# Kernel optimization log

Measured on AMD Instinct MI355X. Metric: run time of the kernel, lower is better.

Reference implementation:

```python
import jax, jax.numpy as jnp
import numpy as np

# graph sizes
N_CLL, B_CLL, NODES_PER_CLL, E_CLL = 120000, 200, 600, 1200000
N_MOL, E_MOL = 64, 256
N_BIO, E_BIO = 19000, 600000
CLL_F, MOL_F, BIO_F = 128, 64, 128
H, MOL_LL, BIO_LL, CLL_LL = 200, 128, 128, 256


def _w(k, shape):
    return jax.random.normal(k, shape, dtype=jnp.float32) * 0.05


def setup_inputs() -> dict:
    key = jax.random.key(0)
    k = jax.random.split(key, 32)
    inp = {
        'x_cll': jax.random.normal(k[0], (N_CLL, CLL_F), dtype=jnp.float32),
        'x_mol': jax.random.normal(k[1], (N_MOL, MOL_F), dtype=jnp.float32),
        'x_bio': jax.random.normal(k[2], (N_BIO, BIO_F), dtype=jnp.float32),
        'edge_cll': jax.random.randint(k[3], (2, E_CLL), 0, N_CLL, dtype=jnp.int32),
        'batch_cll': (jnp.arange(N_CLL, dtype=jnp.int32) // NODES_PER_CLL),
        'edge_mol': jax.random.randint(k[4], (2, E_MOL), 0, N_MOL, dtype=jnp.int32),
        'edge_bio': jax.random.randint(k[5], (2, E_BIO), 0, N_BIO, dtype=jnp.int32),
        # cll branch (GCNConv x2 + Linear)
        'Wc1': _w(k[6], (CLL_F, H)), 'bc1': _w(k[7], (H,)),
        'Wc2': _w(k[8], (H, H)), 'bc2': _w(k[9], (H,)),
        'Wlc': _w(k[10], (H, CLL_LL)), 'blc': _w(k[11], (CLL_LL,)),
        # mol branch (GraphConv x2 + Linear)
        'Wrel1': _w(k[12], (MOL_F, H)), 'brel1': _w(k[13], (H,)), 'Wroot1': _w(k[14], (MOL_F, H)),
        'Wrel2': _w(k[15], (H, H)), 'brel2': _w(k[16], (H,)), 'Wroot2': _w(k[17], (H, H)),
        'Wlm': _w(k[18], (H, MOL_LL)), 'blm': _w(k[19], (MOL_LL,)),
        # bio branch (GCNConv x2 + Linear)
        'Wb1': _w(k[20], (BIO_F, H)), 'bb1': _w(k[21], (H,)),
        'Wb2': _w(k[22], (H, H)), 'bb2': _w(k[23], (H,)),
        'Wlb': _w(k[24], (H, BIO_LL)), 'blb': _w(k[25], (BIO_LL,)),
        # bilinear score
        'W': _w(k[26], (CLL_LL, MOL_LL + BIO_LL)),
        'bias': _w(k[27], (1,)),
    }
    return inp


def gcn_conv(x, src, dst, W, b, n):
    # PyG GCNConv: h = X W; out = D^-1/2 (A+I) D^-1/2 h + b
    h = x @ W
    loop = jnp.arange(n, dtype=src.dtype)
    s = jnp.concatenate([src, loop])
    d = jnp.concatenate([dst, loop])
    deg = jax.ops.segment_sum(jnp.ones(s.shape[0], h.dtype), d, num_segments=n)
    dinv = jax.lax.rsqrt(deg)  # deg >= 1 due to self loops
    norm = dinv[s] * dinv[d]
    return jax.ops.segment_sum(h[s] * norm[:, None], d, num_segments=n) + b


def graph_conv(x, src, dst, Wrel, brel, Wroot, n):
    # PyG GraphConv (aggr='add'): out_i = Wrel * sum_{j->i} x_j + brel + Wroot * x_i
    agg = jax.ops.segment_sum(x[src], dst, num_segments=n)
    return agg @ Wrel + brel + x @ Wroot


def mean_pool(x, batch, num_graphs):
    sums = jax.ops.segment_sum(x, batch, num_segments=num_graphs)
    cnt = jax.ops.segment_sum(jnp.ones(x.shape[0], x.dtype), batch, num_segments=num_graphs)
    return sums / cnt[:, None]


def reference(x_cll, x_mol, x_bio, edge_cll, batch_cll, edge_mol, edge_bio,
              Wc1, bc1, Wc2, bc2, Wlc, blc,
              Wrel1, brel1, Wroot1, Wrel2, brel2, Wroot2, Wlm, blm,
              Wb1, bb1, Wb2, bb2, Wlb, blb, W, bias):
    relu = jax.nn.relu
    # cell-line branch
    h = relu(gcn_conv(x_cll, edge_cll[0], edge_cll[1], Wc1, bc1, N_CLL))
    h = relu(gcn_conv(h, edge_cll[0], edge_cll[1], Wc2, bc2, N_CLL))
    xc = mean_pool(h, batch_cll, B_CLL) @ Wlc + blc  # [B_CLL, CLL_LL]
    # molecule branch (single graph -> batch of 1)
    m = relu(graph_conv(x_mol, edge_mol[0], edge_mol[1], Wrel1, brel1, Wroot1, N_MOL))
    m = relu(graph_conv(m, edge_mol[0], edge_mol[1], Wrel2, brel2, Wroot2, N_MOL))
    xm = jnp.mean(m, axis=0, keepdims=True) @ Wlm + blm  # [1, MOL_LL]
    # bio (PPI) branch: uses only the last node's embedding
    bnodes = relu(gcn_conv(x_bio, edge_bio[0], edge_bio[1], Wb1, bb1, N_BIO))
    bnodes = relu(gcn_conv(bnodes, edge_bio[0], edge_bio[1], Wb2, bb2, N_BIO))
    xb = bnodes[-1].reshape(1, -1) @ Wlb + blb  # [1, BIO_LL]
    # bilinear score
    x_drug = jnp.concatenate([xm, xb], axis=1)  # [1, MOL_LL+BIO_LL]
    scores = (xc @ W) @ x_drug.T + bias  # [B_CLL, 1]
    return scores
```

## Files before the change

### kernel.cpp

```cpp
#include <hip/hip_runtime.h>

typedef unsigned short u16;
typedef __attribute__((ext_vector_type(8))) short s16x8;
typedef __attribute__((ext_vector_type(4))) float f32x4;
typedef __attribute__((ext_vector_type(4))) unsigned u32x4;
typedef __attribute__((ext_vector_type(2))) unsigned u32x2;

#define N_CLLN 120000
#define B_CLLN 200
#define NPG    600
#define E_CLLN 1200000
#define N_MOLN 64
#define E_MOLN 256
#define N_BION 19000
#define E_BION 600000
#define NTOT   (N_CLLN + N_BION)
#define ETOT   (E_CLLN + E_BION)
#define HDIM   200
#define NT     13
#define FCAP   2048

__device__ __forceinline__ float b2f(u16 u){ return __uint_as_float(((unsigned)u)<<16); }
__device__ __forceinline__ float u2f_lo(unsigned u){ return __uint_as_float(u<<16); }
__device__ __forceinline__ float u2f_hi(unsigned u){ return __uint_as_float(u & 0xFFFF0000u); }
__device__ __forceinline__ u16 f2b(float f){
  unsigned x = __float_as_uint(f);
  return (u16)((x + 0x7fffu + ((x>>16)&1u)) >> 16);
}

__global__ void hist_all(const int* __restrict__ eC, const int* __restrict__ eB,
                         int* __restrict__ cnt, int* __restrict__ eidx){
  int i = blockIdx.x*blockDim.x + threadIdx.x;
  if (i < E_CLLN)      eidx[i] = atomicAdd(&cnt[eC[E_CLLN + i]], 1);
  else if (i < ETOT)   eidx[i] = atomicAdd(&cnt[N_CLLN + eB[E_BION + (i - E_CLLN)]], 1);
}
__global__ void make_dinv(const int* __restrict__ cnt, float* __restrict__ dinv, int N){
  int i = blockIdx.x*blockDim.x + threadIdx.x;
  if (i < N) dinv[i] = rsqrtf((float)cnt[i] + 1.0f);
}
__global__ void scan1(const int* __restrict__ cnt, int* __restrict__ rows,
                      int* __restrict__ bsum, int N){
  __shared__ int sh[256];
  int b = blockIdx.x, t = threadIdx.x;
  int base = b*1024 + t*4;
  int v[4]; int s = 0;
#pragma unroll
  for (int i=0;i<4;i++){ int idx = base+i; v[i] = (idx<N)?cnt[idx]:0; s += v[i]; }
  sh[t] = s; __syncthreads();
  for (int off=1; off<256; off<<=1){
    int x = (t>=off)? sh[t-off] : 0; __syncthreads();
    sh[t] += x; __syncthreads();
  }
  int run = (t==0)? 0 : sh[t-1];
#pragma unroll
  for (int i=0;i<4;i++){ int idx = base+i; if (idx<N) rows[idx] = run; run += v[i]; }
  if (t==255) bsum[b] = sh[255];
}
__global__ void scan2(int* __restrict__ bsum, int nb){
  __shared__ int sh[256];
  int t = threadIdx.x;
  sh[t] = (t<nb)? bsum[t] : 0; __syncthreads();
  for (int off=1; off<256; off<<=1){
    int x = (t>=off)? sh[t-off] : 0; __syncthreads();
    sh[t] += x; __syncthreads();
  }
  if (t<nb) bsum[t] = (t==0)? 0 : sh[t-1];
}
__global__ void scan3(int* __restrict__ rows, const int* __restrict__ bsum, int N){
  int i = blockIdx.x*blockDim.x + threadIdx.x;
  if (i<N) rows[i] += bsum[i>>10];
}
__global__ void scatter_all(const int* __restrict__ eC, const int* __restrict__ eB,
                            const int* __restrict__ rows, const int* __restrict__ eidx,
                            int* __restrict__ csr){
  int i = blockIdx.x*blockDim.x + threadIdx.x;
  if (i < E_CLLN){
    int d = eC[E_CLLN + i];
    csr[rows[d] + eidx[i]] = eC[i];
  } else if (i < ETOT){
    int j = i - E_CLLN;
    int d = N_CLLN + eB[E_BION + j];
    csr[rows[d] + eidx[i]] = eB[j];
  }
}

__global__ void prescale128(const float* __restrict__ x, const float* __restrict__ dinv,
                            u16* __restrict__ out, int N){
  int idx = blockIdx.x*blockDim.x + threadIdx.x;
  if (idx >= N*16) return;
  int r = idx >> 4, c8 = (idx & 15) << 3;
  float dv = dinv[r];
  const float* p = x + (size_t)r*128 + c8;
  f32x4 v0 = *(const f32x4*)p;
  f32x4 v1 = *(const f32x4*)(p+4);
  u32x4 w;
  w[0] = (unsigned)f2b(v0[0]*dv) | ((unsigned)f2b(v0[1]*dv)<<16);
  w[1] = (unsigned)f2b(v0[2]*dv) | ((unsigned)f2b(v0[3]*dv)<<16);
  w[2] = (unsigned)f2b(v1[0]*dv) | ((unsigned)f2b(v1[1]*dv)<<16);
  w[3] = (unsigned)f2b(v1[2]*dv) | ((unsigned)f2b(v1[3]*dv)<<16);
  *(u32x4*)(out + (size_t)r*128 + c8) = w;
}

__global__ __launch_bounds__(256) void gather128(
    const u16* __restrict__ X, const float* __restrict__ dinv,
    const int* __restrict__ rows, const int* __restrict__ csr,
    u16* __restrict__ Y, int N, int E)
{
  int wid = (blockIdx.x*blockDim.x + threadIdx.x) >> 6;
  int l = threadIdx.x & 63;
  if (wid >= N) return;
  int half = l >> 5, lh = l & 31;
  float dv = dinv[wid];
  int e0 = rows[wid];
  int e1 = (wid+1 < N) ? rows[wid+1] : E;
  const unsigned* base = (const unsigned*)X;
  float a0=0.f, a1=0.f, a2=0.f, a3=0.f;
  if (half == 0){
    u32x2 sv = *((const u32x2*)(base + (size_t)wid*64) + lh);
    a0 = u2f_lo(sv[0]); a1 = u2f_hi(sv[0]);
    a2 = u2f_lo(sv[1]); a3 = u2f_hi(sv[1]);
  }
  for (int b0 = e0; b0 < e1; b0 += 64){
    int n = e1 - b0;
    int cnt = n < 64 ? n : 64;
    int myv = (l < cnt) ? csr[b0 + l] : 0;
    int i = 0;
    for (; i + 15 < cnt; i += 16){
      u32x2 P[8];
#pragma unroll
      for (int u=0;u<8;u++){
        int s = __shfl(myv, i + 2*u + half);
        P[u] = *((const u32x2*)(base + (size_t)s*64) + lh);
      }
#pragma unroll
      for (int u=0;u<8;u++){
        a0 += u2f_lo(P[u][0]); a1 += u2f_hi(P[u][0]);
        a2 += u2f_lo(P[u][1]); a3 += u2f_hi(P[u][1]);
      }
    }
    for (; i < cnt; i += 2){
      int idx = i + half;
      int cidx = idx < cnt ? idx : cnt-1;
      int s = __shfl(myv, cidx);
      u32x2 P = *((const u32x2*)(base + (size_t)s*64) + lh);
      if (idx < cnt){
        a0 += u2f_lo(P[0]); a1 += u2f_hi(P[0]);
        a2 += u2f_lo(P[1]); a3 += u2f_hi(P[1]);
      }
    }
  }
  a0 += __shfl_xor(a0, 32); a1 += __shfl_xor(a1, 32);
  a2 += __shfl_xor(a2, 32); a3 += __shfl_xor(a3, 32);
  if (half == 0){
    u32x2 wv;
    wv[0] = (unsigned)f2b(a0*dv) | ((unsigned)f2b(a1*dv) << 16);
    wv[1] = (unsigned)f2b(a2*dv) | ((unsigned)f2b(a3*dv) << 16);
    *((u32x2*)((unsigned*)Y + (size_t)wid*64) + lh) = wv;
  }
}

__global__ __launch_bounds__(256) void gather200(
    const u16* __restrict__ t, const float* __restrict__ dinv,
    const int* __restrict__ rows, const int* __restrict__ csr,
    u16* __restrict__ out, int N, int E)
{
  int wid = (blockIdx.x*blockDim.x + threadIdx.x) >> 6;
  int l = threadIdx.x & 63;
  if (wid >= N) return;
  int half = l >> 5, lh = l & 31;
  bool act = lh < 25;
  float dv = dinv[wid];
  int e0 = rows[wid];
  int e1 = (wid+1 < N) ? rows[wid+1] : E;
  const unsigned* base = (const unsigned*)t;
  float a0=0.f,a1=0.f,a2=0.f,a3=0.f,a4=0.f,a5=0.f,a6=0.f,a7=0.f;
  if (half == 0 && act){
    u32x4 sv = *((const u32x4*)(base + (size_t)wid*100) + lh);
    a0 = u2f_lo(sv[0]); a1 = u2f_hi(sv[0]);
    a2 = u2f_lo(sv[1]); a3 = u2f_hi(sv[1]);
    a4 = u2f_lo(sv[2]); a5 = u2f_hi(sv[2]);
    a6 = u2f_lo(sv[3]); a7 = u2f_hi(sv[3]);
  }
  for (int b0 = e0; b0 < e1; b0 += 64){
    int n = e1 - b0;
    int cnt = n < 64 ? n : 64;
    int myv = (l < cnt) ? csr[b0 + l] : 0;
    int i = 0;
    for (; i + 15 < cnt; i += 16){
      int ss[8];
#pragma unroll
      for (int u=0;u<8;u++) ss[u] = __shfl(myv, i + 2*u + half);
      u32x4 P[8];
#pragma unroll
      for (int u=0;u<8;u++){
        u32x4 z = {0,0,0,0};
        P[u] = act ? *((const u32x4*)(base + (size_t)ss[u]*100) + lh) : z;
      }
#pragma unroll
      for (int u=0;u<8;u++){
        a0 += u2f_lo(P[u][0]); a1 += u2f_hi(P[u][0]);
        a2 += u2f_lo(P[u][1]); a3 += u2f_hi(P[u][1]);
        a4 += u2f_lo(P[u][2]); a5 += u2f_hi(P[u][2]);
        a6 += u2f_lo(P[u][3]); a7 += u2f_hi(P[u][3]);
      }
    }
    for (; i < cnt; i += 2){
      int idx = i + half;
      int cidx = idx < cnt ? idx : cnt-1;
      int s = __shfl(myv, cidx);
      u32x4 P = {0,0,0,0};
      if (act) P = *((const u32x4*)(base + (size_t)s*100) + lh);
      if (idx < cnt){
        a0 += u2f_lo(P[0]); a1 += u2f_hi(P[0]);
        a2 += u2f_lo(P[1]); a3 += u2f_hi(P[1]);
        a4 += u2f_lo(P[2]); a5 += u2f_hi(P[2]);
        a6 += u2f_lo(P[3]); a7 += u2f_hi(P[3]);
      }
    }
  }
  a0 += __shfl_xor(a0, 32); a1 += __shfl_xor(a1, 32);
  a2 += __shfl_xor(a2, 32); a3 += __shfl_xor(a3, 32);
  a4 += __shfl_xor(a4, 32); a5 += __shfl_xor(a5, 32);
  a6 += __shfl_xor(a6, 32); a7 += __shfl_xor(a7, 32);
  if (half == 0 && act){
    u32x4 wv;
    wv[0] = (unsigned)f2b(a0*dv) | ((unsigned)f2b(a1*dv) << 16);
    wv[1] = (unsigned)f2b(a2*dv) | ((unsigned)f2b(a3*dv) << 16);
    wv[2] = (unsigned)f2b(a4*dv) | ((unsigned)f2b(a5*dv) << 16);
    wv[3] = (unsigned)f2b(a6*dv) | ((unsigned)f2b(a7*dv) << 16);
    *((u32x4*)((unsigned*)out + (size_t)wid*100) + lh) = wv;
  }
}

__device__ __forceinline__ void pack_one(const float* W, u16* Bp, int K, int idx){
  int l  = idx & 63;
  int nt = (idx >> 6) % NT;
  int kk = idx / (64*NT);
  int n  = nt*16 + (l & 15);
  int k0 = kk*32 + (l>>4)*8;
  u16 v[8];
#pragma unroll
  for (int e=0;e<8;e++){
    int k = k0 + e;
    v[e] = (k < K && n < HDIM) ? f2b(W[(size_t)k*HDIM + n]) : (u16)0;
  }
#pragma unroll
  for (int e=0;e<8;e++) Bp[(size_t)idx*8 + e] = v[e];
}
__global__ void pack_both(const float* __restrict__ Wc1, u16* __restrict__ Pc1,
                          const float* __restrict__ Wc2, u16* __restrict__ Pc2){
  int idx = blockIdx.x*blockDim.x + threadIdx.x;
  const int t1 = 4*NT*64;
  if (idx < t1) pack_one(Wc1, Pc1, 128, idx);
  else if (idx < t1 + 7*NT*64) pack_one(Wc2, Pc2, 200, idx - t1);
}

template<int KSTEPS, int KACT>
__global__ __launch_bounds__(256) void gemm_h1(
    const u16* __restrict__ A, const u16* __restrict__ Bp,
    const float* __restrict__ bias, const float* __restrict__ dinv,
    u16* __restrict__ Out, int M, int Astride)
{
  const int w  = threadIdx.x >> 6;
  const int l  = threadIdx.x & 63;
  const int lm = l & 15;
  const int kg = l >> 4;
  const int base = blockIdx.x*128;
  int r0 = base + w*16 + lm;
  int r1 = r0 + 64;
  const u16* A0 = A + (size_t)(r0 < M ? r0 : 0) * Astride;
  const u16* A1 = A + (size_t)(r1 < M ? r1 : 0) * Astride;
  f32x4 acc[2][NT] = {};
  const s16x8 az = {0,0,0,0,0,0,0,0};
#pragma unroll
  for (int kk=0; kk<KSTEPS; ++kk){
    int k0 = kk*32 + kg*8;
    s16x8 a0 = (k0 < KACT) ? *(const s16x8*)(A0 + k0) : az;
    s16x8 a1 = (k0 < KACT) ? *(const s16x8*)(A1 + k0) : az;
    const u16* bp = Bp + ((size_t)kk*NT*64 + l)*8;
#pragma unroll
    for (int t=0;t<NT;t++){
      s16x8 b = *(const s16x8*)(bp + t*512);
      acc[0][t] = __builtin_amdgcn_mfma_f32_16x16x32_bf16(a0, b, acc[0][t], 0, 0, 0);
      acc[1][t] = __builtin_amdgcn_mfma_f32_16x16x32_bf16(a1, b, acc[1][t], 0, 0, 0);
    }
  }
#pragma unroll
  for (int m=0;m<2;m++){
    int orow = base + m*64 + w*16 + kg*4;
    float scj[4];
#pragma unroll
    for (int j=0;j<4;j++){ int r = orow + j; scj[j] = (r < M) ? dinv[r] : 0.f; }
#pragma unroll
    for (int t=0;t<NT;t++){
      int c = t*16 + lm;
      if (c < HDIM){
#pragma unroll
        for (int j=0;j<4;j++){
          int r = orow + j;
          if (r < M){
            float v = fmaxf(acc[m][t][j] + bias[c], 0.f) * scj[j];
            Out[(size_t)r*HDIM + c] = f2b(v);
          }
        }
      }
    }
  }
}

template<int KSTEPS, int KACT>
__global__ __launch_bounds__(256) void gemm_pool(
    const u16* __restrict__ A, const u16* __restrict__ Bp,
    const float* __restrict__ bias, float* __restrict__ pooled,
    int M, int Astride)
{
  __shared__ float ps[4][2][HDIM+8];
  for (int i = threadIdx.x; i < 4*2*(HDIM+8); i += 256) ((float*)ps)[i] = 0.f;
  __syncthreads();
  const int w  = threadIdx.x >> 6;
  const int l  = threadIdx.x & 63;
  const int lm = l & 15;
  const int kg = l >> 4;
  const int base = blockIdx.x*128;
  int r0 = base + w*16 + lm;
  int r1 = r0 + 64;
  const u16* A0 = A + (size_t)(r0 < M ? r0 : 0) * Astride;
  const u16* A1 = A + (size_t)(r1 < M ? r1 : 0) * Astride;
  f32x4 acc[2][NT] = {};
  const s16x8 az = {0,0,0,0,0,0,0,0};
#pragma unroll
  for (int kk=0; kk<KSTEPS; ++kk){
    int k0 = kk*32 + kg*8;
    s16x8 a0 = (k0 < KACT) ? *(const s16x8*)(A0 + k0) : az;
    s16x8 a1 = (k0 < KACT) ? *(const s16x8*)(A1 + k0) : az;
    const u16* bp = Bp + ((size_t)kk*NT*64 + l)*8;
#pragma unroll
    for (int t=0;t<NT;t++){
      s16x8 b = *(const s16x8*)(bp + t*512);
      acc[0][t] = __builtin_amdgcn_mfma_f32_16x16x32_bf16(a0, b, acc[0][t], 0, 0, 0);
      acc[1][t] = __builtin_amdgcn_mfma_f32_16x16x32_bf16(a1, b, acc[1][t], 0, 0, 0);
    }
  }
  const int g0 = base / NPG;
#pragma unroll
  for (int m=0;m<2;m++){
    int R0 = base + m*64 + w*16;
    bool uni = (R0 + 15 < M) && ((R0/NPG) == ((R0+15)/NPG));
    int slotU = (R0/NPG) - g0;
#pragma unroll
    for (int t=0;t<NT;t++){
      int c = t*16 + lm;
      if (c < HDIM){
        float v0 = fmaxf(acc[m][t][0] + bias[c], 0.f);
        float v1 = fmaxf(acc[m][t][1] + bias[c], 0.f);
        float v2 = fmaxf(acc[m][t][2] + bias[c], 0.f);
        float v3 = fmaxf(acc[m][t][3] + bias[c], 0.f);
        if (uni){
          float s = v0+v1+v2+v3;
          s += __shfl_xor(s, 16);
          s += __shfl_xor(s, 32);
          if (kg == 0) ps[w][slotU][c] += s;
        } else {
          float s0 = 0.f, s1 = 0.f;
          float vv[4] = {v0,v1,v2,v3};
#pragma unroll
          for (int j=0;j<4;j++){
            int r = R0 + kg*4 + j;
            if (r < M){
              if ((r/NPG) - g0 == 0) s0 += vv[j]; else s1 += vv[j];
            }
          }
          s0 += __shfl_xor(s0, 16); s0 += __shfl_xor(s0, 32);
          s1 += __shfl_xor(s1, 16); s1 += __shfl_xor(s1, 32);
          if (kg == 0){ ps[w][0][c] += s0; ps[w][1][c] += s1; }
        }
      }
    }
  }
  __syncthreads();
  for (int i = threadIdx.x; i < 2*HDIM; i += 256){
    int slot = i / HDIM, c = i % HDIM;
    float s = ps[0][slot][c] + ps[1][slot][c] + ps[2][slot][c] + ps[3][slot][c];
    int g = g0 + slot;
    if (g < B_CLLN && s != 0.f) unsafeAtomicAdd(&pooled[g*HDIM + c], s);
  }
}

__global__ void xc_kernel(const float* __restrict__ pooled, const float* __restrict__ Wlc,
                          const float* __restrict__ blc, float* __restrict__ xc){
  __shared__ float p[HDIM];
  int b = blockIdx.x, j = threadIdx.x;
  if (j < HDIM) p[j] = pooled[b*HDIM + j] * (1.0f/NPG);
  __syncthreads();
  float s = blc[j];
  for (int k=0;k<HDIM;k++) s += p[k]*Wlc[(size_t)k*256 + j];
  xc[(size_t)b*256 + j] = s;
}

__global__ void bio_front(const float* __restrict__ x_bio, const float* __restrict__ dinvAll,
                          const int* __restrict__ rowAll, const int* __restrict__ csr,
                          float* __restrict__ Y1f, float* __restrict__ dvF){
  const float* dinvB = dinvAll + N_CLLN;
  int g0l = rowAll[NTOT - 1];
  int fcnt = (ETOT - g0l) + 1; if (fcnt > FCAP) fcnt = FCAP;
  int wid = (blockIdx.x*blockDim.x + threadIdx.x) >> 6;
  int nw  = (gridDim.x*blockDim.x) >> 6;
  int l = threadIdx.x & 63;
  for (int k = wid; k < fcnt; k += nw){
    int v = (k == 0) ? (N_BION - 1) : csr[g0l + k - 1];
    float dv = dinvB[v];
    int e0 = rowAll[N_CLLN + v];
    int e1 = (v + 1 < N_BION) ? rowAll[N_CLLN + v + 1] : ETOT;
    float c0 = x_bio[(size_t)v*128 + l]      * dv;
    float c1 = x_bio[(size_t)v*128 + l + 64] * dv;
    for (int e = e0; e < e1; ++e){
      int s = csr[e];
      float ds = dinvB[s];
      c0 += x_bio[(size_t)s*128 + l]      * ds;
      c1 += x_bio[(size_t)s*128 + l + 64] * ds;
    }
    Y1f[(size_t)k*128 + l]      = c0 * dv;
    Y1f[(size_t)k*128 + l + 64] = c1 * dv;
    if (l == 0) dvF[k] = dv;
  }
}

__global__ __launch_bounds__(256) void bio_h1acc(
    const float* __restrict__ Y1f, const float* __restrict__ dvF,
    const int* __restrict__ rowAll,
    const float* __restrict__ Wb1, const float* __restrict__ bb1,
    float* __restrict__ Y2acc){
  __shared__ float y1[128];
  int tid = threadIdx.x;
  int g0l = rowAll[NTOT - 1];
  int fcnt = (ETOT - g0l) + 1; if (fcnt > FCAP) fcnt = FCAP;
  for (int k = blockIdx.x; k < fcnt; k += gridDim.x){
    if (tid < 128) y1[tid] = Y1f[(size_t)k*128 + tid];
    __syncthreads();
    if (tid < HDIM){
      float s = bb1[tid];
#pragma unroll 8
      for (int q=0;q<128;q++) s += y1[q]*Wb1[q*HDIM + tid];
      unsafeAtomicAdd(&Y2acc[tid], fmaxf(s, 0.f)*dvF[k]);
    }
    __syncthreads();
  }
}

__global__ void bio_fin(const float* __restrict__ Y2acc, const float* __restrict__ dinvAll,
                        const float* __restrict__ Wb2, const float* __restrict__ bb2,
                        const float* __restrict__ Wlb, const float* __restrict__ blb,
                        float* __restrict__ xb){
  __shared__ float Y2[HDIM];
  __shared__ float wv[HDIM];
  int tid = threadIdx.x;
  float dl = dinvAll[NTOT - 1];
  if (tid < HDIM) Y2[tid] = Y2acc[tid] * dl;
  __syncthreads();
  if (tid < HDIM){
    float s = bb2[tid];
#pragma unroll 8
    for (int q=0;q<HDIM;q++) s += Y2[q]*Wb2[q*HDIM + tid];
    wv[tid] = fmaxf(s, 0.f);
  }
  __syncthreads();
  if (tid < 128){
    float s = blb[tid];
#pragma unroll 8
    for (int c=0;c<HDIM;c++) s += wv[c]*Wlb[c*128 + tid];
    xb[tid] = s;
  }
}

__global__ void mol_agg(const float* __restrict__ x, const int* __restrict__ src,
                        const int* __restrict__ dst, float* __restrict__ a, int E, int F){
  int idx = blockIdx.x*blockDim.x + threadIdx.x;
  if (idx >= E*F) return;
  int e = idx / F, f = idx % F;
  unsafeAtomicAdd(&a[dst[e]*F + f], x[(size_t)src[e]*F + f]);
}
__global__ void mol_l1(const float* __restrict__ x, const float* __restrict__ a1,
                       const float* __restrict__ Wrel, const float* __restrict__ brel,
                       const float* __restrict__ Wroot, float* __restrict__ m1){
  int idx = blockIdx.x*blockDim.x + threadIdx.x;
  if (idx >= N_MOLN*HDIM) return;
  int i = idx / HDIM, c = idx % HDIM;
  float s = brel[c];
  for (int k=0;k<64;k++){
    s += a1[i*64+k]*Wrel[k*HDIM+c];
    s += x[i*64+k]*Wroot[k*HDIM+c];
  }
  m1[idx] = fmaxf(s, 0.f);
}
__global__ void mol_l2(const float* __restrict__ m1, const float* __restrict__ a2,
                       const float* __restrict__ Wrel2, const float* __restrict__ brel2,
                       const float* __restrict__ Wroot2, float* __restrict__ colsum){
  int idx = blockIdx.x*blockDim.x + threadIdx.x;
  if (idx >= N_MOLN*HDIM) return;
  int i = idx / HDIM, c = idx % HDIM;
  float s = brel2[c];
  for (int k=0;k<HDIM;k++){
    s += a2[i*HDIM+k]*Wrel2[k*HDIM+c] + m1[i*HDIM+k]*Wroot2[k*HDIM+c];
  }
  s = fmaxf(s, 0.f);
  unsafeAtomicAdd(&colsum[c], s*(1.0f/N_MOLN));
}
__global__ void mol_head(const float* __restrict__ colsum, const float* __restrict__ Wlm,
                         const float* __restrict__ blm, float* __restrict__ xm){
  int j = threadIdx.x;
  if (j >= 128) return;
  float s = blm[j];
  for (int c=0;c<HDIM;c++) s += colsum[c]*Wlm[c*128+j];
  xm[j] = s;
}

__global__ void score_kernel(const float* __restrict__ xc, const float* __restrict__ W,
                             const float* __restrict__ bias, const float* __restrict__ xm,
                             const float* __restrict__ xb, float* __restrict__ out){
  __shared__ float xd[256];
  __shared__ float u[256];
  int tid = threadIdx.x;
  xd[tid] = (tid < 128) ? xm[tid] : xb[tid-128];
  __syncthreads();
  float s = 0.f;
  for (int j=0;j<256;j++) s += W[(size_t)tid*256 + j]*xd[j];
  u[tid] = s;
  __syncthreads();
  if (tid < B_CLLN){
    float sc = bias[0];
    const float* xr = xc + (size_t)tid*256;
    for (int i=0;i<256;i++) sc += xr[i]*u[i];
    out[tid] = sc;
  }
}

extern "C" void kernel_launch(void* const* d_in, const int* in_sizes, int n_in,
                              void* d_out, int out_size, void* d_ws, size_t ws_size,
                              hipStream_t stream) {
  const float* x_cll = (const float*)d_in[0];
  const float* x_mol = (const float*)d_in[1];
  const float* x_bio = (const float*)d_in[2];
  const int* e_cll = (const int*)d_in[3];
  const int* e_mol = (const int*)d_in[5];
  const int* e_bio = (const int*)d_in[6];
  const float *Wc1=(const float*)d_in[7],  *bc1=(const float*)d_in[8];
  const float *Wc2=(const float*)d_in[9],  *bc2=(const float*)d_in[10];
  const float *Wlc=(const float*)d_in[11], *blc=(const float*)d_in[12];
  const float *Wrel1=(const float*)d_in[13],*brel1=(const float*)d_in[14],*Wroot1=(const float*)d_in[15];
  const float *Wrel2=(const float*)d_in[16],*brel2=(const float*)d_in[17],*Wroot2=(const float*)d_in[18];
  const float *Wlm=(const float*)d_in[19], *blm=(const float*)d_in[20];
  const float *Wb1=(const float*)d_in[21], *bb1=(const float*)d_in[22];
  const float *Wb2=(const float*)d_in[23], *bb2=(const float*)d_in[24];
  const float *Wlb=(const float*)d_in[25], *blb=(const float*)d_in[26];
  const float *Wbl=(const float*)d_in[27], *bias=(const float*)d_in[28];
  float* out = (float*)d_out;

  char* ws = (char*)d_ws;
  size_t o = 0;
  auto alloc = [&](size_t bytes)->char*{
    char* p = ws + o;
    o = (o + bytes + 255) & ~(size_t)255;
    return p;
  };
  u16*   XS    = (u16*)  alloc((size_t)N_CLLN*128*2);
  u16*   Y1    = (u16*)  alloc((size_t)N_CLLN*128*2);
  u16*   BUF1  = (u16*)  alloc((size_t)N_CLLN*HDIM*2 + 512);
  u16*   BUF2  = (u16*)  alloc((size_t)N_CLLN*HDIM*2 + 512);
  float* dinvA = (float*)alloc((size_t)NTOT*4);
  int*   cntA  = (int*)  alloc((size_t)NTOT*4);
  int*   rowA  = (int*)  alloc((size_t)NTOT*4);
  int*   csrA  = (int*)  alloc((size_t)ETOT*4);
  int*   eidx  = (int*)  alloc((size_t)ETOT*4);
  int*   bsum  = (int*)  alloc(256*4);
  float* pooled= (float*)alloc((size_t)B_CLLN*HDIM*4);
  float* xc    = (float*)alloc((size_t)B_CLLN*256*4);
  float* a1    = (float*)alloc((size_t)(N_MOLN*64 + N_MOLN*HDIM + 2*HDIM)*4);
  float* a2    = a1 + N_MOLN*64;
  float* colsum= a2 + N_MOLN*HDIM;
  float* Y2acc = colsum + HDIM;
  float* m1    = (float*)alloc((size_t)N_MOLN*HDIM*4);
  float* xm    = (float*)alloc(128*4);
  float* xb    = (float*)alloc(128*4);
  float* Y1f   = (float*)alloc((size_t)FCAP*128*4);
  float* dvF   = (float*)alloc((size_t)FCAP*4);
  u16* Pc1 = (u16*)alloc((size_t)4*NT*64*8*2);
  u16* Pc2 = (u16*)alloc((size_t)7*NT*64*8*2);
  if (o > ws_size) return;
  (void)in_sizes; (void)n_in; (void)out_size;

  hipMemsetAsync(cntA, 0, (size_t)NTOT*4, stream);
  hipMemsetAsync(pooled, 0, (size_t)B_CLLN*HDIM*4, stream);
  hipMemsetAsync(a1, 0, (size_t)(N_MOLN*64 + N_MOLN*HDIM + 2*HDIM)*4, stream);

  pack_both<<<(11*NT*64+255)/256, 256, 0, stream>>>(Wc1, Pc1, Wc2, Pc2);

  hist_all<<<(ETOT+255)/256, 256, 0, stream>>>(e_cll, e_bio, cntA, eidx);
  make_dinv<<<(NTOT+255)/256, 256, 0, stream>>>(cntA, dinvA, NTOT);
  scan1<<<(NTOT+1023)/1024, 256, 0, stream>>>(cntA, rowA, bsum, NTOT);
  scan2<<<1, 256, 0, stream>>>(bsum, (NTOT+1023)/1024);
  scan3<<<(NTOT+255)/256, 256, 0, stream>>>(rowA, bsum, NTOT);
  scatter_all<<<(ETOT+255)/256, 256, 0, stream>>>(e_cll, e_bio, rowA, eidx, csrA);

  const int wcll = (N_CLLN+3)/4;
  const int mcll = (N_CLLN+127)/128;

  prescale128<<<(N_CLLN*16+255)/256, 256, 0, stream>>>(x_cll, dinvA, XS, N_CLLN);
  gather128<<<wcll, 256, 0, stream>>>(XS, dinvA, rowA, csrA, Y1, N_CLLN, E_CLLN);
  gemm_h1<4,128><<<mcll, 256, 0, stream>>>(Y1, Pc1, bc1, dinvA, BUF1, N_CLLN, 128);
  gather200<<<wcll, 256, 0, stream>>>(BUF1, dinvA, rowA, csrA, BUF2, N_CLLN, E_CLLN);
  gemm_pool<7,200><<<mcll, 256, 0, stream>>>(BUF2, Pc2, bc2, pooled, N_CLLN, HDIM);
  xc_kernel<<<B_CLLN, 256, 0, stream>>>(pooled, Wlc, blc, xc);

  bio_front<<<16, 256, 0, stream>>>(x_bio, dinvA, rowA, csrA, Y1f, dvF);
  bio_h1acc<<<64, 256, 0, stream>>>(Y1f, dvF, rowA, Wb1, bb1, Y2acc);
  bio_fin<<<1, 256, 0, stream>>>(Y2acc, dinvA, Wb2, bb2, Wlb, blb, xb);

  mol_agg<<<(E_MOLN*64+255)/256, 256, 0, stream>>>(x_mol, e_mol, e_mol + E_MOLN, a1, E_MOLN, 64);
  mol_l1<<<(N_MOLN*HDIM+255)/256, 256, 0, stream>>>(x_mol, a1, Wrel1, brel1, Wroot1, m1);
  mol_agg<<<(E_MOLN*HDIM+255)/256, 256, 0, stream>>>(m1, e_mol, e_mol + E_MOLN, a2, E_MOLN, HDIM);
  mol_l2<<<(N_MOLN*HDIM+255)/256, 256, 0, stream>>>(m1, a2, Wrel2, brel2, Wroot2, colsum);
  mol_head<<<1, 128, 0, stream>>>(colsum, Wlm, blm, xm);

  score_kernel<<<1, 256, 0, stream>>>(xc, Wbl, bias, xm, xb, out);
}
```

Baseline: 512.2 us.

## Fuse neighbor gather with MFMA GEMM via shared-memory tiles for cell-line layers

Each cell-line GCN layer's CSR gather is merged into its MFMA GEMM kernel. A block of four waves gathers 64 node rows into an LDS tile and then multiplies that tile by the packed weights, so the intermediate Y1 and BUF2 arrays are no longer written to and read back from global memory. The dinv computation is also folded into scan1, which removes one launch. In exchange, each block now covers 64 rows instead of 128, so weight loads are reused less. The per-wave serial gather loop over 16 nodes, followed by a barrier, may also reduce latency hiding compared with the separate gather kernels.

```diff
diff --git a/kernel.cpp b/kernel.cpp
--- a/kernel.cpp
+++ b/kernel.cpp
@@ -19,6 +19,8 @@
 #define HDIM   200
 #define NT     13
 #define FCAP   2048
+#define ST1    136
+#define ST2    216
 
 __device__ __forceinline__ float b2f(u16 u){ return __uint_as_float(((unsigned)u)<<16); }
 __device__ __forceinline__ float u2f_lo(unsigned u){ return __uint_as_float(u<<16); }
@@ -34,18 +36,19 @@
   if (i < E_CLLN)      eidx[i] = atomicAdd(&cnt[eC[E_CLLN + i]], 1);
   else if (i < ETOT)   eidx[i] = atomicAdd(&cnt[N_CLLN + eB[E_BION + (i - E_CLLN)]], 1);
 }
-__global__ void make_dinv(const int* __restrict__ cnt, float* __restrict__ dinv, int N){
-  int i = blockIdx.x*blockDim.x + threadIdx.x;
-  if (i < N) dinv[i] = rsqrtf((float)cnt[i] + 1.0f);
-}
-__global__ void scan1(const int* __restrict__ cnt, int* __restrict__ rows,
-                      int* __restrict__ bsum, int N){
+__global__ void scan1(const int* __restrict__ cnt, float* __restrict__ dinv,
+                      int* __restrict__ rows, int* __restrict__ bsum, int N){
   __shared__ int sh[256];
   int b = blockIdx.x, t = threadIdx.x;
   int base = b*1024 + t*4;
   int v[4]; int s = 0;
 #pragma unroll
-  for (int i=0;i<4;i++){ int idx = base+i; v[i] = (idx<N)?cnt[idx]:0; s += v[i]; }
+  for (int i=0;i<4;i++){
+    int idx = base+i;
+    v[i] = (idx<N)?cnt[idx]:0;
+    if (idx<N) dinv[idx] = rsqrtf((float)v[i] + 1.0f);
+    s += v[i];
+  }
   sh[t] = s; __syncthreads();
   for (int off=1; off<256; off<<=1){
     int x = (t>=off)? sh[t-off] : 0; __syncthreads();
@@ -101,137 +104,6 @@
   *(u32x4*)(out + (size_t)r*128 + c8) = w;
 }
 
-__global__ __launch_bounds__(256) void gather128(
-    const u16* __restrict__ X, const float* __restrict__ dinv,
-    const int* __restrict__ rows, const int* __restrict__ csr,
-    u16* __restrict__ Y, int N, int E)
-{
-  int wid = (blockIdx.x*blockDim.x + threadIdx.x) >> 6;
-  int l = threadIdx.x & 63;
-  if (wid >= N) return;
-  int half = l >> 5, lh = l & 31;
-  float dv = dinv[wid];
-  int e0 = rows[wid];
-  int e1 = (wid+1 < N) ? rows[wid+1] : E;
-  const unsigned* base = (const unsigned*)X;
-  float a0=0.f, a1=0.f, a2=0.f, a3=0.f;
-  if (half == 0){
-    u32x2 sv = *((const u32x2*)(base + (size_t)wid*64) + lh);
-    a0 = u2f_lo(sv[0]); a1 = u2f_hi(sv[0]);
-    a2 = u2f_lo(sv[1]); a3 = u2f_hi(sv[1]);
-  }
-  for (int b0 = e0; b0 < e1; b0 += 64){
-    int n = e1 - b0;
-    int cnt = n < 64 ? n : 64;
-    int myv = (l < cnt) ? csr[b0 + l] : 0;
-    int i = 0;
-    for (; i + 15 < cnt; i += 16){
-      u32x2 P[8];
-#pragma unroll
-      for (int u=0;u<8;u++){
-        int s = __shfl(myv, i + 2*u + half);
-        P[u] = *((const u32x2*)(base + (size_t)s*64) + lh);
-      }
-#pragma unroll
-      for (int u=0;u<8;u++){
-        a0 += u2f_lo(P[u][0]); a1 += u2f_hi(P[u][0]);
-        a2 += u2f_lo(P[u][1]); a3 += u2f_hi(P[u][1]);
-      }
-    }
-    for (; i < cnt; i += 2){
-      int idx = i + half;
-      int cidx = idx < cnt ? idx : cnt-1;
-      int s = __shfl(myv, cidx);
-      u32x2 P = *((const u32x2*)(base + (size_t)s*64) + lh);
-      if (idx < cnt){
-        a0 += u2f_lo(P[0]); a1 += u2f_hi(P[0]);
-        a2 += u2f_lo(P[1]); a3 += u2f_hi(P[1]);
-      }
-    }
-  }
-  a0 += __shfl_xor(a0, 32); a1 += __shfl_xor(a1, 32);
-  a2 += __shfl_xor(a2, 32); a3 += __shfl_xor(a3, 32);
-  if (half == 0){
-    u32x2 wv;
-    wv[0] = (unsigned)f2b(a0*dv) | ((unsigned)f2b(a1*dv) << 16);
-    wv[1] = (unsigned)f2b(a2*dv) | ((unsigned)f2b(a3*dv) << 16);
-    *((u32x2*)((unsigned*)Y + (size_t)wid*64) + lh) = wv;
-  }
-}
-
-__global__ __launch_bounds__(256) void gather200(
-    const u16* __restrict__ t, const float* __restrict__ dinv,
-    const int* __restrict__ rows, const int* __restrict__ csr,
-    u16* __restrict__ out, int N, int E)
-{
-  int wid = (blockIdx.x*blockDim.x + threadIdx.x) >> 6;
-  int l = threadIdx.x & 63;
-  if (wid >= N) return;
-  int half = l >> 5, lh = l & 31;
-  bool act = lh < 25;
-  float dv = dinv[wid];
-  int e0 = rows[wid];
-  int e1 = (wid+1 < N) ? rows[wid+1] : E;
-  const unsigned* base = (const unsigned*)t;
-  float a0=0.f,a1=0.f,a2=0.f,a3=0.f,a4=0.f,a5=0.f,a6=0.f,a7=0.f;
-  if (half == 0 && act){
-    u32x4 sv = *((const u32x4*)(base + (size_t)wid*100) + lh);
-    a0 = u2f_lo(sv[0]); a1 = u2f_hi(sv[0]);
-    a2 = u2f_lo(sv[1]); a3 = u2f_hi(sv[1]);
-    a4 = u2f_lo(sv[2]); a5 = u2f_hi(sv[2]);
-    a6 = u2f_lo(sv[3]); a7 = u2f_hi(sv[3]);
-  }
-  for (int b0 = e0; b0 < e1; b0 += 64){
-    int n = e1 - b0;
-    int cnt = n < 64 ? n : 64;
-    int myv = (l < cnt) ? csr[b0 + l] : 0;
-    int i = 0;
-    for (; i + 15 < cnt; i += 16){
-      int ss[8];
-#pragma unroll
-      for (int u=0;u<8;u++) ss[u] = __shfl(myv, i + 2*u + half);
-      u32x4 P[8];
-#pragma unroll
-      for (int u=0;u<8;u++){
-        u32x4 z = {0,0,0,0};
-        P[u] = act ? *((const u32x4*)(base + (size_t)ss[u]*100) + lh) : z;
-      }
-#pragma unroll
-      for (int u=0;u<8;u++){
-        a0 += u2f_lo(P[u][0]); a1 += u2f_hi(P[u][0]);
-        a2 += u2f_lo(P[u][1]); a3 += u2f_hi(P[u][1]);
-        a4 += u2f_lo(P[u][2]); a5 += u2f_hi(P[u][2]);
-        a6 += u2f_lo(P[u][3]); a7 += u2f_hi(P[u][3]);
-      }
-    }
-    for (; i < cnt; i += 2){
-      int idx = i + half;
-      int cidx = idx < cnt ? idx : cnt-1;
-      int s = __shfl(myv, cidx);
-      u32x4 P = {0,0,0,0};
-      if (act) P = *((const u32x4*)(base + (size_t)s*100) + lh);
-      if (idx < cnt){
-        a0 += u2f_lo(P[0]); a1 += u2f_hi(P[0]);
-        a2 += u2f_lo(P[1]); a3 += u2f_hi(P[1]);
-        a4 += u2f_lo(P[2]); a5 += u2f_hi(P[2]);
-        a6 += u2f_lo(P[3]); a7 += u2f_hi(P[3]);
-      }
-    }
-  }
-  a0 += __shfl_xor(a0, 32); a1 += __shfl_xor(a1, 32);
-  a2 += __shfl_xor(a2, 32); a3 += __shfl_xor(a3, 32);
-  a4 += __shfl_xor(a4, 32); a5 += __shfl_xor(a5, 32);
-  a6 += __shfl_xor(a6, 32); a7 += __shfl_xor(a7, 32);
-  if (half == 0 && act){
-    u32x4 wv;
-    wv[0] = (unsigned)f2b(a0*dv) | ((unsigned)f2b(a1*dv) << 16);
-    wv[1] = (unsigned)f2b(a2*dv) | ((unsigned)f2b(a3*dv) << 16);
-    wv[2] = (unsigned)f2b(a4*dv) | ((unsigned)f2b(a5*dv) << 16);
-    wv[3] = (unsigned)f2b(a6*dv) | ((unsigned)f2b(a7*dv) << 16);
-    *((u32x4*)((unsigned*)out + (size_t)wid*100) + lh) = wv;
-  }
-}
-
 __device__ __forceinline__ void pack_one(const float* W, u16* Bp, int K, int idx){
   int l  = idx & 63;
   int nt = (idx >> 6) % NT;
@@ -255,125 +127,227 @@
   else if (idx < t1 + 7*NT*64) pack_one(Wc2, Pc2, 200, idx - t1);
 }
 
-template<int KSTEPS, int KACT>
-__global__ __launch_bounds__(256) void gemm_h1(
-    const u16* __restrict__ A, const u16* __restrict__ Bp,
-    const float* __restrict__ bias, const float* __restrict__ dinv,
-    u16* __restrict__ Out, int M, int Astride)
+__global__ __launch_bounds__(256) void fused_h1(
+    const u16* __restrict__ XS, const float* __restrict__ dinv,
+    const int* __restrict__ rows, const int* __restrict__ csr,
+    const u16* __restrict__ Bp, const float* __restrict__ bias,
+    u16* __restrict__ Out, int M, int E)
 {
-  const int w  = threadIdx.x >> 6;
-  const int l  = threadIdx.x & 63;
-  const int lm = l & 15;
-  const int kg = l >> 4;
-  const int base = blockIdx.x*128;
-  int r0 = base + w*16 + lm;
-  int r1 = r0 + 64;
-  const u16* A0 = A + (size_t)(r0 < M ? r0 : 0) * Astride;
-  const u16* A1 = A + (size_t)(r1 < M ? r1 : 0) * Astride;
-  f32x4 acc[2][NT] = {};
-  const s16x8 az = {0,0,0,0,0,0,0,0};
-#pragma unroll
-  for (int kk=0; kk<KSTEPS; ++kk){
-    int k0 = kk*32 + kg*8;
-    s16x8 a0 = (k0 < KACT) ? *(const s16x8*)(A0 + k0) : az;
-    s16x8 a1 = (k0 < KACT) ? *(const s16x8*)(A1 + k0) : az;
+  __shared__ u16 tile[64*ST1];
+  const int w = threadIdx.x >> 6;
+  const int l = threadIdx.x & 63;
+  const int half = l >> 5, lh = l & 31;
+  const int lm = l & 15, kg = l >> 4;
+  const int base = blockIdx.x*64;
+  const unsigned* srcb = (const unsigned*)XS;
+  for (int r = 0; r < 16; ++r){
+    int node = base + w*16 + r;
+    int nc = node < M ? node : M-1;
+    float dv = dinv[nc];
+    int e0 = rows[nc];
+    int e1 = (nc+1 < M) ? rows[nc+1] : E;
+    float a0=0.f, a1=0.f, a2=0.f, a3=0.f;
+    if (half == 0){
+      u32x2 sv = *((const u32x2*)(srcb + (size_t)nc*64) + lh);
+      a0 = u2f_lo(sv[0]); a1 = u2f_hi(sv[0]);
+      a2 = u2f_lo(sv[1]); a3 = u2f_hi(sv[1]);
+    }
+    for (int b0 = e0; b0 < e1; b0 += 64){
+      int n = e1 - b0;
+      int cnt = n < 64 ? n : 64;
+      int myv = (l < cnt) ? csr[b0 + l] : 0;
+      int i = 0;
+      for (; i + 15 < cnt; i += 16){
+        u32x2 P[8];
+#pragma unroll
+        for (int u=0;u<8;u++){
+          int s = __shfl(myv, i + 2*u + half);
+          P[u] = *((const u32x2*)(srcb + (size_t)s*64) + lh);
+        }
+#pragma unroll
+        for (int u=0;u<8;u++){
+          a0 += u2f_lo(P[u][0]); a1 += u2f_hi(P[u][0]);
+          a2 += u2f_lo(P[u][1]); a3 += u2f_hi(P[u][1]);
+        }
+      }
+      for (; i < cnt; i += 2){
+        int idx = i + half;
+        int ci = idx < cnt ? idx : cnt-1;
+        int s = __shfl(myv, ci);
+        u32x2 P = *((const u32x2*)(srcb + (size_t)s*64) + lh);
+        if (idx < cnt){
+          a0 += u2f_lo(P[0]); a1 += u2f_hi(P[0]);
+          a2 += u2f_lo(P[1]); a3 += u2f_hi(P[1]);
+        }
+      }
+    }
+    a0 += __shfl_xor(a0, 32); a1 += __shfl_xor(a1, 32);
+    a2 += __shfl_xor(a2, 32); a3 += __shfl_xor(a3, 32);
+    if (half == 0){
+      u32x2 wv;
+      wv[0] = (unsigned)f2b(a0*dv) | ((unsigned)f2b(a1*dv) << 16);
+      wv[1] = (unsigned)f2b(a2*dv) | ((unsigned)f2b(a3*dv) << 16);
+      *((u32x2*)((unsigned*)(tile + (size_t)(w*16+r)*ST1)) + lh) = wv;
+    }
+  }
+  __syncthreads();
+  f32x4 acc[NT] = {};
+  const u16* Arow = tile + (size_t)(w*16 + lm)*ST1;
+#pragma unroll
+  for (int kk=0; kk<4; ++kk){
+    s16x8 a = *(const s16x8*)(Arow + kk*32 + kg*8);
     const u16* bp = Bp + ((size_t)kk*NT*64 + l)*8;
 #pragma unroll
     for (int t=0;t<NT;t++){
       s16x8 b = *(const s16x8*)(bp + t*512);
-      acc[0][t] = __builtin_amdgcn_mfma_f32_16x16x32_bf16(a0, b, acc[0][t], 0, 0, 0);
-      acc[1][t] = __builtin_amdgcn_mfma_f32_16x16x32_bf16(a1, b, acc[1][t], 0, 0, 0);
-    }
-  }
-#pragma unroll
-  for (int m=0;m<2;m++){
-    int orow = base + m*64 + w*16 + kg*4;
-    float scj[4];
-#pragma unroll
-    for (int j=0;j<4;j++){ int r = orow + j; scj[j] = (r < M) ? dinv[r] : 0.f; }
-#pragma unroll
-    for (int t=0;t<NT;t++){
-      int c = t*16 + lm;
-      if (c < HDIM){
-#pragma unroll
-        for (int j=0;j<4;j++){
-          int r = orow + j;
-          if (r < M){
-            float v = fmaxf(acc[m][t][j] + bias[c], 0.f) * scj[j];
-            Out[(size_t)r*HDIM + c] = f2b(v);
-          }
+      acc[t] = __builtin_amdgcn_mfma_f32_16x16x32_bf16(a, b, acc[t], 0, 0, 0);
+    }
+  }
+  int orow = base + w*16 + kg*4;
+  float scj[4];
+#pragma unroll
+  for (int j=0;j<4;j++){ int r = orow + j; scj[j] = (r < M) ? dinv[r] : 0.f; }
+#pragma unroll
+  for (int t=0;t<NT;t++){
+    int c = t*16 + lm;
+    if (c < HDIM){
+#pragma unroll
+      for (int j=0;j<4;j++){
+        int r = orow + j;
+        if (r < M){
+          float v = fmaxf(acc[t][j] + bias[c], 0.f) * scj[j];
+          Out[(size_t)r*HDIM + c] = f2b(v);
         }
       }
     }
   }
 }
 
-template<int KSTEPS, int KACT>
-__global__ __launch_bounds__(256) void gemm_pool(
-    const u16* __restrict__ A, const u16* __restrict__ Bp,
-    const float* __restrict__ bias, float* __restrict__ pooled,
-    int M, int Astride)
+__global__ __launch_bounds__(256) void fused_pool(
+    const u16* __restrict__ H1, const float* __restrict__ dinv,
+    const int* __restrict__ rows, const int* __restrict__ csr,
+    const u16* __restrict__ Bp, const float* __restrict__ bias,
+    float* __restrict__ pooled, int M, int E)
 {
+  __shared__ u16 tile[64*ST2];
   __shared__ float ps[4][2][HDIM+8];
   for (int i = threadIdx.x; i < 4*2*(HDIM+8); i += 256) ((float*)ps)[i] = 0.f;
-  __syncthreads();
-  const int w  = threadIdx.x >> 6;
-  const int l  = threadIdx.x & 63;
-  const int lm = l & 15;
-  const int kg = l >> 4;
-  const int base = blockIdx.x*128;
-  int r0 = base + w*16 + lm;
-  int r1 = r0 + 64;
-  const u16* A0 = A + (size_t)(r0 < M ? r0 : 0) * Astride;
-  const u16* A1 = A + (size_t)(r1 < M ? r1 : 0) * Astride;
-  f32x4 acc[2][NT] = {};
+  const int w = threadIdx.x >> 6;
+  const int l = threadIdx.x & 63;
+  const int half = l >> 5, lh = l & 31;
+  const int lm = l & 15, kg = l >> 4;
+  const bool act = lh < 25;
+  const int base = blockIdx.x*64;
+  const unsigned* srcb = (const unsigned*)H1;
+  for (int r = 0; r < 16; ++r){
+    int node = base + w*16 + r;
+    int nc = node < M ? node : M-1;
+    float dv = dinv[nc];
+    int e0 = rows[nc];
+    int e1 = (nc+1 < M) ? rows[nc+1] : E;
+    float a0=0.f,a1=0.f,a2=0.f,a3=0.f,a4=0.f,a5=0.f,a6=0.f,a7=0.f;
+    if (half == 0 && act){
+      u32x4 sv = *((const u32x4*)(srcb + (size_t)nc*100) + lh);
+      a0 = u2f_lo(sv[0]); a1 = u2f_hi(sv[0]);
+      a2 = u2f_lo(sv[1]); a3 = u2f_hi(sv[1]);
+      a4 = u2f_lo(sv[2]); a5 = u2f_hi(sv[2]);
+      a6 = u2f_lo(sv[3]); a7 = u2f_hi(sv[3]);
+    }
+    for (int b0 = e0; b0 < e1; b0 += 64){
+      int n = e1 - b0;
+      int cnt = n < 64 ? n : 64;
+      int myv = (l < cnt) ? csr[b0 + l] : 0;
+      int i = 0;
+      for (; i + 15 < cnt; i += 16){
+        int ss[8];
+#pragma unroll
+        for (int u=0;u<8;u++) ss[u] = __shfl(myv, i + 2*u + half);
+        u32x4 P[8];
+#pragma unroll
+        for (int u=0;u<8;u++){
+          u32x4 z = {0,0,0,0};
+          P[u] = act ? *((const u32x4*)(srcb + (size_t)ss[u]*100) + lh) : z;
+        }
+#pragma unroll
+        for (int u=0;u<8;u++){
+          a0 += u2f_lo(P[u][0]); a1 += u2f_hi(P[u][0]);
+          a2 += u2f_lo(P[u][1]); a3 += u2f_hi(P[u][1]);
+          a4 += u2f_lo(P[u][2]); a5 += u2f_hi(P[u][2]);
+          a6 += u2f_lo(P[u][3]); a7 += u2f_hi(P[u][3]);
+        }
+      }
+      for (; i < cnt; i += 2){
+        int idx = i + half;
+        int ci = idx < cnt ? idx : cnt-1;
+        int s = __shfl(myv, ci);
+        u32x4 P = {0,0,0,0};
+        if (act) P = *((const u32x4*)(srcb + (size_t)s*100) + lh);
+        if (idx < cnt){
+          a0 += u2f_lo(P[0]); a1 += u2f_hi(P[0]);
+          a2 += u2f_lo(P[1]); a3 += u2f_hi(P[1]);
+          a4 += u2f_lo(P[2]); a5 += u2f_hi(P[2]);
+          a6 += u2f_lo(P[3]); a7 += u2f_hi(P[3]);
+        }
+      }
+    }
+    a0 += __shfl_xor(a0, 32); a1 += __shfl_xor(a1, 32);
+    a2 += __shfl_xor(a2, 32); a3 += __shfl_xor(a3, 32);
+    a4 += __shfl_xor(a4, 32); a5 += __shfl_xor(a5, 32);
+    a6 += __shfl_xor(a6, 32); a7 += __shfl_xor(a7, 32);
+    if (half == 0 && act){
+      u32x4 wv;
+      wv[0] = (unsigned)f2b(a0*dv) | ((unsigned)f2b(a1*dv) << 16);
+      wv[1] = (unsigned)f2b(a2*dv) | ((unsigned)f2b(a3*dv) << 16);
+      wv[2] = (unsigned)f2b(a4*dv) | ((unsigned)f2b(a5*dv) << 16);
+      wv[3] = (unsigned)f2b(a6*dv) | ((unsigned)f2b(a7*dv) << 16);
+      *((u32x4*)((unsigned*)(tile + (size_t)(w*16+r)*ST2)) + lh) = wv;
+    }
+  }
+  __syncthreads();
+  f32x4 acc[NT] = {};
   const s16x8 az = {0,0,0,0,0,0,0,0};
-#pragma unroll
-  for (int kk=0; kk<KSTEPS; ++kk){
+  const u16* Arow = tile + (size_t)(w*16 + lm)*ST2;
+#pragma unroll
+  for (int kk=0; kk<7; ++kk){
     int k0 = kk*32 + kg*8;
-    s16x8 a0 = (k0 < KACT) ? *(const s16x8*)(A0 + k0) : az;
-    s16x8 a1 = (k0 < KACT) ? *(const s16x8*)(A1 + k0) : az;
+    s16x8 a = (k0 < HDIM) ? *(const s16x8*)(Arow + k0) : az;
     const u16* bp = Bp + ((size_t)kk*NT*64 + l)*8;
 #pragma unroll
     for (int t=0;t<NT;t++){
       s16x8 b = *(const s16x8*)(bp + t*512);
-      acc[0][t] = __builtin_amdgcn_mfma_f32_16x16x32_bf16(a0, b, acc[0][t], 0, 0, 0);
-      acc[1][t] = __builtin_amdgcn_mfma_f32_16x16x32_bf16(a1, b, acc[1][t], 0, 0, 0);
+      acc[t] = __builtin_amdgcn_mfma_f32_16x16x32_bf16(a, b, acc[t], 0, 0, 0);
     }
   }
   const int g0 = base / NPG;
-#pragma unroll
-  for (int m=0;m<2;m++){
-    int R0 = base + m*64 + w*16;
-    bool uni = (R0 + 15 < M) && ((R0/NPG) == ((R0+15)/NPG));
-    int slotU = (R0/NPG) - g0;
-#pragma unroll
-    for (int t=0;t<NT;t++){
-      int c = t*16 + lm;
-      if (c < HDIM){
-        float v0 = fmaxf(acc[m][t][0] + bias[c], 0.f);
-        float v1 = fmaxf(acc[m][t][1] + bias[c], 0.f);
-        float v2 = fmaxf(acc[m][t][2] + bias[c], 0.f);
-        float v3 = fmaxf(acc[m][t][3] + bias[c], 0.f);
-        if (uni){
-          float s = v0+v1+v2+v3;
-          s += __shfl_xor(s, 16);
-          s += __shfl_xor(s, 32);
-          if (kg == 0) ps[w][slotU][c] += s;
-        } else {
-          float s0 = 0.f, s1 = 0.f;
-          float vv[4] = {v0,v1,v2,v3};
-#pragma unroll
-          for (int j=0;j<4;j++){
-            int r = R0 + kg*4 + j;
-            if (r < M){
-              if ((r/NPG) - g0 == 0) s0 += vv[j]; else s1 += vv[j];
-            }
+  int R0 = base + w*16;
+  bool uni = (R0 + 15 < M) && ((R0/NPG) == ((R0+15)/NPG));
+  int slotU = (R0/NPG) - g0;
+#pragma unroll
+  for (int t=0;t<NT;t++){
+    int c = t*16 + lm;
+    if (c < HDIM){
+      float v0 = fmaxf(acc[t][0] + bias[c], 0.f);
+      float v1 = fmaxf(acc[t][1] + bias[c], 0.f);
+      float v2 = fmaxf(acc[t][2] + bias[c], 0.f);
+      float v3 = fmaxf(acc[t][3] + bias[c], 0.f);
+      if (uni){
+        float s = v0+v1+v2+v3;
+        s += __shfl_xor(s, 16);
+        s += __shfl_xor(s, 32);
+        if (kg == 0) ps[w][slotU][c] += s;
+      } else {
+        float s0 = 0.f, s1 = 0.f;
+        float vv[4] = {v0,v1,v2,v3};
+#pragma unroll
+        for (int j=0;j<4;j++){
+          int r = R0 + kg*4 + j;
+          if (r < M){
+            if ((r/NPG) - g0 == 0) s0 += vv[j]; else s1 += vv[j];
           }
-          s0 += __shfl_xor(s0, 16); s0 += __shfl_xor(s0, 32);
-          s1 += __shfl_xor(s1, 16); s1 += __shfl_xor(s1, 32);
-          if (kg == 0){ ps[w][0][c] += s0; ps[w][1][c] += s1; }
-        }
+        }
+        s0 += __shfl_xor(s0, 16); s0 += __shfl_xor(s0, 32);
+        s1 += __shfl_xor(s1, 16); s1 += __shfl_xor(s1, 32);
+        if (kg == 0){ ps[w][0][c] += s0; ps[w][1][c] += s1; }
       }
     }
   }
@@ -563,9 +537,7 @@
     return p;
   };
   u16*   XS    = (u16*)  alloc((size_t)N_CLLN*128*2);
-  u16*   Y1    = (u16*)  alloc((size_t)N_CLLN*128*2);
   u16*   BUF1  = (u16*)  alloc((size_t)N_CLLN*HDIM*2 + 512);
-  u16*   BUF2  = (u16*)  alloc((size_t)N_CLLN*HDIM*2 + 512);
   float* dinvA = (float*)alloc((size_t)NTOT*4);
   int*   cntA  = (int*)  alloc((size_t)NTOT*4);
   int*   rowA  = (int*)  alloc((size_t)NTOT*4);
@@ -595,20 +567,16 @@
   pack_both<<<(11*NT*64+255)/256, 256, 0, stream>>>(Wc1, Pc1, Wc2, Pc2);
 
   hist_all<<<(ETOT+255)/256, 256, 0, stream>>>(e_cll, e_bio, cntA, eidx);
-  make_dinv<<<(NTOT+255)/256, 256, 0, stream>>>(cntA, dinvA, NTOT);
-  scan1<<<(NTOT+1023)/1024, 256, 0, stream>>>(cntA, rowA, bsum, NTOT);
+  scan1<<<(NTOT+1023)/1024, 256, 0, stream>>>(cntA, dinvA, rowA, bsum, NTOT);
   scan2<<<1, 256, 0, stream>>>(bsum, (NTOT+1023)/1024);
   scan3<<<(NTOT+255)/256, 256, 0, stream>>>(rowA, bsum, NTOT);
   scatter_all<<<(ETOT+255)/256, 256, 0, stream>>>(e_cll, e_bio, rowA, eidx, csrA);
 
-  const int wcll = (N_CLLN+3)/4;
-  const int mcll = (N_CLLN+127)/128;
+  const int fcll = (N_CLLN+63)/64;
 
   prescale128<<<(N_CLLN*16+255)/256, 256, 0, stream>>>(x_cll, dinvA, XS, N_CLLN);
-  gather128<<<wcll, 256, 0, stream>>>(XS, dinvA, rowA, csrA, Y1, N_CLLN, E_CLLN);
-  gemm_h1<4,128><<<mcll, 256, 0, stream>>>(Y1, Pc1, bc1, dinvA, BUF1, N_CLLN, 128);
-  gather200<<<wcll, 256, 0, stream>>>(BUF1, dinvA, rowA, csrA, BUF2, N_CLLN, E_CLLN);
-  gemm_pool<7,200><<<mcll, 256, 0, stream>>>(BUF2, Pc2, bc2, pooled, N_CLLN, HDIM);
+  fused_h1<<<fcll, 256, 0, stream>>>(XS, dinvA, rowA, csrA, Pc1, bc1, BUF1, N_CLLN, E_CLLN);
+  fused_pool<<<fcll, 256, 0, stream>>>(BUF1, dinvA, rowA, csrA, Pc2, bc2, pooled, N_CLLN, E_CLLN);
   xc_kernel<<<B_CLLN, 256, 0, stream>>>(pooled, Wlc, blc, xc);
 
   bio_front<<<16, 256, 0, stream>>>(x_bio, dinvA, rowA, csrA, Y1f, dvF);
```

Result: slower. 600.2 us (+17.2%).
